# Performance work log

Measured on AMD Instinct MI355X. Metric: run time of the kernel, lower is better.

## Reference

```python
import jax, jax.numpy as jnp
import numpy as np

N_NODES = 50000
N_EDGES = 800000
NODE_IN = 16
EDGE_IN = 3
G_DIM = 8
LATENT = 128
NODE_OUT = 1
EDGE_OUT = 1


def _dense_init(key, fan_in, fan_out):
    # flax default: lecun_normal weights, zero bias
    w = jax.random.normal(key, (fan_in, fan_out), jnp.float32) / jnp.sqrt(float(fan_in))
    b = jnp.zeros((fan_out,), jnp.float32)
    return w, b


def setup_inputs() -> dict:
    key = jax.random.key(0)
    ks = jax.random.split(key, 12)
    nodes = jax.random.normal(ks[0], (N_NODES, NODE_IN), jnp.float32)
    edges = jax.random.normal(ks[1], (N_EDGES, EDGE_IN), jnp.float32)
    globals_ = jax.random.normal(ks[2], (1, G_DIM), jnp.float32)
    senders = jax.random.randint(ks[3], (N_EDGES,), 0, N_NODES, jnp.int32)
    receivers = jax.random.randint(ks[4], (N_EDGES,), 0, N_NODES, jnp.int32)
    W_en, b_en = _dense_init(ks[5], NODE_IN, LATENT)      # encoder node Dense
    W_ee, b_ee = _dense_init(ks[6], EDGE_IN, LATENT)      # encoder edge Dense
    mlp_in = 3 * LATENT + G_DIM                           # concat(nodes, sent, recv, globals)
    W1, b1 = _dense_init(ks[7], mlp_in, LATENT)           # node MLP layer 1 (relu)
    W2, b2 = _dense_init(ks[8], LATENT, LATENT)           # node MLP layer 2
    W_dn, b_dn = _dense_init(ks[9], LATENT, NODE_OUT)     # decoder node Dense
    W_de, b_de = _dense_init(ks[10], LATENT, EDGE_OUT)    # decoder edge Dense
    return dict(nodes=nodes, edges=edges, globals_=globals_, senders=senders,
                receivers=receivers, W_en=W_en, b_en=b_en, W_ee=W_ee, b_ee=b_ee,
                W1=W1, b1=b1, W2=W2, b2=b2, W_dn=W_dn, b_dn=b_dn, W_de=W_de, b_de=b_de)


def reference(nodes, edges, globals_, senders, receivers,
              W_en, b_en, W_ee, b_ee, W1, b1, W2, b2, W_dn, b_dn, W_de, b_de):
    n = nodes.shape[0]
    # Encoder (GraphMapFeatures)
    h_n = nodes @ W_en + b_en                     # [N, L]
    h_e = edges @ W_ee + b_ee                     # [E, L]
    # One jraph.GraphNetwork step, update_edge_fn=None -> edges unchanged.
    # sent/received aggregation = segment_sum of edge features by sender/receiver.
    sent = jax.ops.segment_sum(h_e, senders, num_segments=n)      # [N, L]
    recv = jax.ops.segment_sum(h_e, receivers, num_segments=n)    # [N, L]
    gbc = jnp.broadcast_to(globals_[0], (n, globals_.shape[1]))   # single graph
    x = jnp.concatenate((h_n, sent, recv, gbc), axis=1)           # [N, 3L+G]
    x = jax.nn.relu(x @ W1 + b1)
    h_n = x @ W2 + b2
    # update_global_fn reconstructs concat([time], static) == globals (identity).
    # Decoder
    nodes_out = h_n @ W_dn + b_dn                 # [N, 1]
    edges_out = h_e @ W_de + b_de                 # [E, 1]
    return nodes_out, edges_out
```

## Files before the change

kernel.cpp:

```cpp
#include <hip/hip_runtime.h>

#define N_NODES 50000
#define N_EDGES 800000

#define ESR_OFF    0
#define CONSTS_OFF 400000
#define SCAL_OFF   404096
#define PART_OFF   404608

#define NBINS      25
#define BINSZ      2000
#define MAX_CHUNKS 20

__global__ void precompute_kernel(
    const float* __restrict__ g,
    const float* __restrict__ W_en,
    const float* __restrict__ b_en,
    const float* __restrict__ W_ee,
    const float* __restrict__ b_ee,
    const float* __restrict__ W1,
    const float* __restrict__ b1,
    const float* __restrict__ W2,
    const float* __restrict__ b2,
    const float* __restrict__ W_dn,
    const float* __restrict__ b_dn,
    const float* __restrict__ W_de,
    const float* __restrict__ b_de,
    float* __restrict__ ws)
{
    const int s = blockIdx.x;
    const int k = threadIdx.x;
    float* consts = ws + CONSTS_OFF;
    float* scal   = ws + SCAL_OFF;

    if (s < 16) {
        float acc = 0.f;
        for (int l = 0; l < 128; ++l)
            acc += W_en[s * 128 + l] * W1[l * 128 + k];
        consts[k * 32 + s] = acc;
    } else if (s < 19) {
        const int j = s - 16;
        float acc = 0.f;
        for (int l = 0; l < 128; ++l)
            acc += W_ee[j * 128 + l] * W1[(128 + l) * 128 + k];
        consts[k * 32 + s] = acc;
    } else if (s < 22) {
        const int j = s - 19;
        float acc = 0.f;
        for (int l = 0; l < 128; ++l)
            acc += W_ee[j * 128 + l] * W1[(256 + l) * 128 + k];
        consts[k * 32 + s] = acc;
    } else if (s == 22) {
        float acc = b1[k];
        for (int l = 0; l < 128; ++l)
            acc += b_en[l] * W1[l * 128 + k];
        for (int j = 0; j < 8; ++j)
            acc += g[j] * W1[(384 + j) * 128 + k];
        consts[k * 32 + 22] = acc;
    } else if (s == 23) {
        float acc = 0.f;
        for (int l = 0; l < 128; ++l)
            acc += b_ee[l] * W1[(128 + l) * 128 + k];
        consts[k * 32 + 23] = acc;
    } else if (s == 24) {
        float acc = 0.f;
        for (int l = 0; l < 128; ++l)
            acc += b_ee[l] * W1[(256 + l) * 128 + k];
        consts[k * 32 + 24] = acc;
    } else if (s == 25) {
        float acc = 0.f;
        for (int j = 0; j < 128; ++j)
            acc += W2[k * 128 + j] * W_dn[j];
        consts[k * 32 + 25] = acc;
        consts[k * 32 + 26] = 0.f;
        consts[k * 32 + 27] = 0.f;
    } else {
        if (k == 0) {
            float c = b_dn[0];
            for (int j = 0; j < 128; ++j) c += b2[j] * W_dn[j];
            scal[0] = c;
            float ce = b_de[0];
            for (int l = 0; l < 128; ++l) ce += b_ee[l] * W_de[l];
            scal[1] = ce;
            scal[5] = 0.f; scal[6] = 0.f; scal[7] = 0.f;
        }
        if (k < 3) {
            float acc = 0.f;
            for (int l = 0; l < 128; ++l)
                acc += W_ee[k * 128 + l] * W_de[l];
            scal[2 + k] = acc;
        }
    }
}

__global__ __launch_bounds__(256) void edge_out_kernel(
    const float* __restrict__ edges,
    const float* __restrict__ ws,
    float* __restrict__ out_edges)
{
    const int e4 = (blockIdx.x * 256 + threadIdx.x) * 4;
    if (e4 >= N_EDGES) return;
    const float* scal = ws + SCAL_OFF;
    const float w0 = scal[2], w1 = scal[3], w2 = scal[4], cb = scal[1];
    const float4* ep = (const float4*)(edges + (size_t)e4 * 3);
    const float4 f0 = ep[0], f1 = ep[1], f2 = ep[2];
    float4 o;
    o.x = fmaf(f0.x, w0, fmaf(f0.y, w1, fmaf(f0.z, w2, cb)));
    o.y = fmaf(f0.w, w0, fmaf(f1.x, w1, fmaf(f1.y, w2, cb)));
    o.z = fmaf(f1.z, w0, fmaf(f1.w, w1, fmaf(f2.x, w2, cb)));
    o.w = fmaf(f2.y, w0, fmaf(f2.z, w1, fmaf(f2.w, w2, cb)));
    *(float4*)(out_edges + e4) = o;
}

__global__ __launch_bounds__(512) void agg_kernel(
    const float* __restrict__ edges,
    const int*   __restrict__ senders,
    const int*   __restrict__ receivers,
    float* __restrict__ ws,
    int ce)
{
    __shared__ float4 acc4[BINSZ * 2];
    float* acc = (float*)acc4;
    const int tid = threadIdx.x;
    for (int i = tid; i < BINSZ * 2; i += 512)
        acc4[i] = make_float4(0.f, 0.f, 0.f, 0.f);
    __syncthreads();

    const int chunk = blockIdx.x;
    const int bin   = blockIdx.y;
    const int lo    = bin * BINSZ;

    const int e_beg = chunk * ce;
    const int e_end = min(e_beg + ce, N_EDGES);
    for (int e4 = e_beg + tid * 4; e4 < e_end; e4 += 512 * 4) {
        const int4 s4 = *(const int4*)(senders + e4);
        const int4 r4 = *(const int4*)(receivers + e4);
        const unsigned ds0 = (unsigned)(s4.x - lo), ds1 = (unsigned)(s4.y - lo);
        const unsigned ds2 = (unsigned)(s4.z - lo), ds3 = (unsigned)(s4.w - lo);
        const unsigned dr0 = (unsigned)(r4.x - lo), dr1 = (unsigned)(r4.y - lo);
        const unsigned dr2 = (unsigned)(r4.z - lo), dr3 = (unsigned)(r4.w - lo);
        const bool h = (ds0 < BINSZ) | (ds1 < BINSZ) | (ds2 < BINSZ) | (ds3 < BINSZ) |
                       (dr0 < BINSZ) | (dr1 < BINSZ) | (dr2 < BINSZ) | (dr3 < BINSZ);
        if (!h) continue;
        const float4* ep = (const float4*)(edges + (size_t)e4 * 3);
        const float4 f0 = ep[0], f1 = ep[1], f2 = ep[2];
        if (ds0 < BINSZ) {
            atomicAdd(&acc[ds0 * 8 + 0], f0.x); atomicAdd(&acc[ds0 * 8 + 1], f0.y);
            atomicAdd(&acc[ds0 * 8 + 2], f0.z); atomicAdd(&acc[ds0 * 8 + 3], 1.0f);
        }
        if (dr0 < BINSZ) {
            atomicAdd(&acc[dr0 * 8 + 4], f0.x); atomicAdd(&acc[dr0 * 8 + 5], f0.y);
            atomicAdd(&acc[dr0 * 8 + 6], f0.z); atomicAdd(&acc[dr0 * 8 + 7], 1.0f);
        }
        if (ds1 < BINSZ) {
            atomicAdd(&acc[ds1 * 8 + 0], f0.w); atomicAdd(&acc[ds1 * 8 + 1], f1.x);
            atomicAdd(&acc[ds1 * 8 + 2], f1.y); atomicAdd(&acc[ds1 * 8 + 3], 1.0f);
        }
        if (dr1 < BINSZ) {
            atomicAdd(&acc[dr1 * 8 + 4], f0.w); atomicAdd(&acc[dr1 * 8 + 5], f1.x);
            atomicAdd(&acc[dr1 * 8 + 6], f1.y); atomicAdd(&acc[dr1 * 8 + 7], 1.0f);
        }
        if (ds2 < BINSZ) {
            atomicAdd(&acc[ds2 * 8 + 0], f1.z); atomicAdd(&acc[ds2 * 8 + 1], f1.w);
            atomicAdd(&acc[ds2 * 8 + 2], f2.x); atomicAdd(&acc[ds2 * 8 + 3], 1.0f);
        }
        if (dr2 < BINSZ) {
            atomicAdd(&acc[dr2 * 8 + 4], f1.z); atomicAdd(&acc[dr2 * 8 + 5], f1.w);
            atomicAdd(&acc[dr2 * 8 + 6], f2.x); atomicAdd(&acc[dr2 * 8 + 7], 1.0f);
        }
        if (ds3 < BINSZ) {
            atomicAdd(&acc[ds3 * 8 + 0], f2.y); atomicAdd(&acc[ds3 * 8 + 1], f2.z);
            atomicAdd(&acc[ds3 * 8 + 2], f2.w); atomicAdd(&acc[ds3 * 8 + 3], 1.0f);
        }
        if (dr3 < BINSZ) {
            atomicAdd(&acc[dr3 * 8 + 4], f2.y); atomicAdd(&acc[dr3 * 8 + 5], f2.z);
            atomicAdd(&acc[dr3 * 8 + 6], f2.w); atomicAdd(&acc[dr3 * 8 + 7], 1.0f);
        }
    }
    __syncthreads();

    float4* dst = (float4*)(ws + PART_OFF + (size_t)chunk * (N_NODES * 8) + (size_t)lo * 8);
    for (int i = tid; i < BINSZ * 2; i += 512)
        dst[i] = acc4[i];
}

__global__ __launch_bounds__(256) void edge_kernel_atomic(
    const float* __restrict__ edges,
    const int*   __restrict__ senders,
    const int*   __restrict__ receivers,
    float* __restrict__ ws)
{
    const int e = blockIdx.x * 256 + threadIdx.x;
    if (e >= N_EDGES) return;
    const float e0 = edges[e * 3 + 0];
    const float e1 = edges[e * 3 + 1];
    const float e2 = edges[e * 3 + 2];
    const int s = senders[e];
    const int r = receivers[e];
    float* esr = ws + ESR_OFF;
    atomicAdd(&esr[s * 8 + 0], e0);
    atomicAdd(&esr[s * 8 + 1], e1);
    atomicAdd(&esr[s * 8 + 2], e2);
    atomicAdd(&esr[s * 8 + 3], 1.0f);
    atomicAdd(&esr[r * 8 + 4], e0);
    atomicAdd(&esr[r * 8 + 5], e1);
    atomicAdd(&esr[r * 8 + 6], e2);
    atomicAdd(&esr[r * 8 + 7], 1.0f);
}

__global__ __launch_bounds__(256) void node_kernel(
    const float* __restrict__ nodes,
    const float* __restrict__ ws,
    float* __restrict__ out_nodes,
    int nchunks)
{
    __shared__ float4 lds4[128 * 8];
    const float4* consts4 = (const float4*)(ws + CONSTS_OFF);
    for (int i = threadIdx.x; i < 128 * 8; i += 256)
        lds4[i] = consts4[i];
    __syncthreads();

    const int n = blockIdx.x * 256 + threadIdx.x;
    if (n >= N_NODES) return;

    const float4* np4 = (const float4*)(nodes + (size_t)n * 16);
    const float4 n0 = np4[0], n1 = np4[1], n2 = np4[2], n3 = np4[3];

    float4 es = make_float4(0.f, 0.f, 0.f, 0.f);
    float4 er = make_float4(0.f, 0.f, 0.f, 0.f);
    if (nchunks > 0) {
        for (int c = 0; c < nchunks; ++c) {
            const float4* p = (const float4*)(ws + PART_OFF + (size_t)c * (N_NODES * 8) + (size_t)n * 8);
            const float4 a = p[0], b = p[1];
            es.x += a.x; es.y += a.y; es.z += a.z; es.w += a.w;
            er.x += b.x; er.y += b.y; er.z += b.z; er.w += b.w;
        }
    } else {
        const float4* p = (const float4*)(ws + ESR_OFF + (size_t)n * 8);
        es = p[0];
        er = p[1];
    }

    float acc = 0.f;
#pragma unroll 4
    for (int k = 0; k < 128; ++k) {
        const float4* c4 = &lds4[k * 8];
        const float4 m0 = c4[0], m1 = c4[1], m2 = c4[2], m3 = c4[3];
        const float4 q0 = c4[4];
        const float4 q1 = c4[5];
        const float4 q2 = c4[6];
        float pre = q1.z
            + n0.x * m0.x + n0.y * m0.y + n0.z * m0.z + n0.w * m0.w
            + n1.x * m1.x + n1.y * m1.y + n1.z * m1.z + n1.w * m1.w
            + n2.x * m2.x + n2.y * m2.y + n2.z * m2.z + n2.w * m2.w
            + n3.x * m3.x + n3.y * m3.y + n3.z * m3.z + n3.w * m3.w
            + es.x * q0.x + es.y * q0.y + es.z * q0.z
            + er.x * q0.w + er.y * q1.x + er.z * q1.y
            + es.w * q1.w + er.w * q2.x;
        acc += fmaxf(pre, 0.f) * q2.y;
    }
    const float* scal = ws + SCAL_OFF;
    out_nodes[n] = acc + scal[0];
}

extern "C" void kernel_launch(void* const* d_in, const int* in_sizes, int n_in,
                              void* d_out, int out_size, void* d_ws, size_t ws_size,
                              hipStream_t stream) {
    const float* nodes     = (const float*)d_in[0];
    const float* edges     = (const float*)d_in[1];
    const float* globals_  = (const float*)d_in[2];
    const int*   senders   = (const int*)d_in[3];
    const int*   receivers = (const int*)d_in[4];
    const float* W_en = (const float*)d_in[5];
    const float* b_en = (const float*)d_in[6];
    const float* W_ee = (const float*)d_in[7];
    const float* b_ee = (const float*)d_in[8];
    const float* W1   = (const float*)d_in[9];
    const float* b1   = (const float*)d_in[10];
    const float* W2   = (const float*)d_in[11];
    const float* b2   = (const float*)d_in[12];
    const float* W_dn = (const float*)d_in[13];
    const float* b_dn = (const float*)d_in[14];
    const float* W_de = (const float*)d_in[15];
    const float* b_de = (const float*)d_in[16];

    float* ws = (float*)d_ws;
    float* out = (float*)d_out;

    precompute_kernel<<<27, 128, 0, stream>>>(
        globals_, W_en, b_en, W_ee, b_ee, W1, b1, W2, b2,
        W_dn, b_dn, W_de, b_de, ws);

    edge_out_kernel<<<(N_EDGES / 4 + 255) / 256, 256, 0, stream>>>(
        edges, ws, out + N_NODES);

    long ws_floats = (long)(ws_size / 4);
    long avail = (ws_floats - PART_OFF) / (N_NODES * 8);
    int nchunks = (int)(avail < 0 ? 0 : (avail > MAX_CHUNKS ? MAX_CHUNKS : avail));

    if (nchunks >= 1) {
        int ce = (N_EDGES + nchunks - 1) / nchunks;
        ce = (ce + 3) & ~3;
        dim3 grid(nchunks, NBINS);
        agg_kernel<<<grid, 512, 0, stream>>>(edges, senders, receivers, ws, ce);
    } else {
        hipMemsetAsync(ws + ESR_OFF, 0, (size_t)N_NODES * 8 * sizeof(float), stream);
        edge_kernel_atomic<<<(N_EDGES + 255) / 256, 256, 0, stream>>>(
            edges, senders, receivers, ws);
    }

    node_kernel<<<(N_NODES + 255) / 256, 256, 0, stream>>>(
        nodes, ws, out, nchunks);
}
```

Before: 175.1 us.

## Split aggregation into separate sender and receiver bins with larger LDS bins

The aggregation kernel now gives sender and receiver scatter each their own blocks. Each block reads only one index array and accumulates 4 floats per node instead of 8, which lets a bin cover 4000 nodes in the same LDS footprint. The partial buffers are split into separate sender and receiver arrays, and the per-thread step grows to 8 edges. The point is to cut the number of bins each block must scan and the redundant index reads. In exchange, edge features are now read by both the sender and receiver passes, and the node-range check for the last partial bin has to be handled at write-out.

```diff
diff --git a/kernel.cpp b/kernel.cpp
--- a/kernel.cpp
+++ b/kernel.cpp
@@ -8,8 +8,8 @@
 #define SCAL_OFF   404096
 #define PART_OFF   404608
 
-#define NBINS      25
-#define BINSZ      2000
+#define NBINS      13
+#define BINSZ      4000
 #define MAX_CHUNKS 20
 
 __global__ void precompute_kernel(
@@ -116,71 +116,80 @@
     const float* __restrict__ edges,
     const int*   __restrict__ senders,
     const int*   __restrict__ receivers,
-    float* __restrict__ ws,
+    float* __restrict__ part_s,
+    float* __restrict__ part_r,
     int ce)
 {
-    __shared__ float4 acc4[BINSZ * 2];
+    __shared__ float4 acc4[BINSZ];
     float* acc = (float*)acc4;
     const int tid = threadIdx.x;
-    for (int i = tid; i < BINSZ * 2; i += 512)
+    for (int i = tid; i < BINSZ; i += 512)
         acc4[i] = make_float4(0.f, 0.f, 0.f, 0.f);
     __syncthreads();
 
-    const int chunk = blockIdx.x;
-    const int bin   = blockIdx.y;
-    const int lo    = bin * BINSZ;
+    const int chunk  = blockIdx.x;
+    const int binid  = blockIdx.y;
+    const bool is_s  = binid < NBINS;
+    const int bin    = is_s ? binid : binid - NBINS;
+    const int lo     = bin * BINSZ;
+    const int* __restrict__ idx = is_s ? senders : receivers;
 
     const int e_beg = chunk * ce;
     const int e_end = min(e_beg + ce, N_EDGES);
-    for (int e4 = e_beg + tid * 4; e4 < e_end; e4 += 512 * 4) {
-        const int4 s4 = *(const int4*)(senders + e4);
-        const int4 r4 = *(const int4*)(receivers + e4);
-        const unsigned ds0 = (unsigned)(s4.x - lo), ds1 = (unsigned)(s4.y - lo);
-        const unsigned ds2 = (unsigned)(s4.z - lo), ds3 = (unsigned)(s4.w - lo);
-        const unsigned dr0 = (unsigned)(r4.x - lo), dr1 = (unsigned)(r4.y - lo);
-        const unsigned dr2 = (unsigned)(r4.z - lo), dr3 = (unsigned)(r4.w - lo);
-        const bool h = (ds0 < BINSZ) | (ds1 < BINSZ) | (ds2 < BINSZ) | (ds3 < BINSZ) |
-                       (dr0 < BINSZ) | (dr1 < BINSZ) | (dr2 < BINSZ) | (dr3 < BINSZ);
-        if (!h) continue;
-        const float4* ep = (const float4*)(edges + (size_t)e4 * 3);
-        const float4 f0 = ep[0], f1 = ep[1], f2 = ep[2];
-        if (ds0 < BINSZ) {
-            atomicAdd(&acc[ds0 * 8 + 0], f0.x); atomicAdd(&acc[ds0 * 8 + 1], f0.y);
-            atomicAdd(&acc[ds0 * 8 + 2], f0.z); atomicAdd(&acc[ds0 * 8 + 3], 1.0f);
-        }
-        if (dr0 < BINSZ) {
-            atomicAdd(&acc[dr0 * 8 + 4], f0.x); atomicAdd(&acc[dr0 * 8 + 5], f0.y);
-            atomicAdd(&acc[dr0 * 8 + 6], f0.z); atomicAdd(&acc[dr0 * 8 + 7], 1.0f);
-        }
-        if (ds1 < BINSZ) {
-            atomicAdd(&acc[ds1 * 8 + 0], f0.w); atomicAdd(&acc[ds1 * 8 + 1], f1.x);
-            atomicAdd(&acc[ds1 * 8 + 2], f1.y); atomicAdd(&acc[ds1 * 8 + 3], 1.0f);
-        }
-        if (dr1 < BINSZ) {
-            atomicAdd(&acc[dr1 * 8 + 4], f0.w); atomicAdd(&acc[dr1 * 8 + 5], f1.x);
-            atomicAdd(&acc[dr1 * 8 + 6], f1.y); atomicAdd(&acc[dr1 * 8 + 7], 1.0f);
-        }
-        if (ds2 < BINSZ) {
-            atomicAdd(&acc[ds2 * 8 + 0], f1.z); atomicAdd(&acc[ds2 * 8 + 1], f1.w);
-            atomicAdd(&acc[ds2 * 8 + 2], f2.x); atomicAdd(&acc[ds2 * 8 + 3], 1.0f);
-        }
-        if (dr2 < BINSZ) {
-            atomicAdd(&acc[dr2 * 8 + 4], f1.z); atomicAdd(&acc[dr2 * 8 + 5], f1.w);
-            atomicAdd(&acc[dr2 * 8 + 6], f2.x); atomicAdd(&acc[dr2 * 8 + 7], 1.0f);
-        }
-        if (ds3 < BINSZ) {
-            atomicAdd(&acc[ds3 * 8 + 0], f2.y); atomicAdd(&acc[ds3 * 8 + 1], f2.z);
-            atomicAdd(&acc[ds3 * 8 + 2], f2.w); atomicAdd(&acc[ds3 * 8 + 3], 1.0f);
-        }
-        if (dr3 < BINSZ) {
-            atomicAdd(&acc[dr3 * 8 + 4], f2.y); atomicAdd(&acc[dr3 * 8 + 5], f2.z);
-            atomicAdd(&acc[dr3 * 8 + 6], f2.w); atomicAdd(&acc[dr3 * 8 + 7], 1.0f);
+    for (int e8 = e_beg + tid * 8; e8 < e_end; e8 += 512 * 8) {
+        const int4 ia = *(const int4*)(idx + e8);
+        const int4 ib = *(const int4*)(idx + e8 + 4);
+        const unsigned d0 = (unsigned)(ia.x - lo), d1 = (unsigned)(ia.y - lo);
+        const unsigned d2 = (unsigned)(ia.z - lo), d3 = (unsigned)(ia.w - lo);
+        const unsigned d4 = (unsigned)(ib.x - lo), d5 = (unsigned)(ib.y - lo);
+        const unsigned d6 = (unsigned)(ib.z - lo), d7 = (unsigned)(ib.w - lo);
+        if ((d0 < BINSZ) | (d1 < BINSZ) | (d2 < BINSZ) | (d3 < BINSZ)) {
+            const float4* ep = (const float4*)(edges + (size_t)e8 * 3);
+            const float4 f0 = ep[0], f1 = ep[1], f2 = ep[2];
+            if (d0 < BINSZ) {
+                atomicAdd(&acc[d0 * 4 + 0], f0.x); atomicAdd(&acc[d0 * 4 + 1], f0.y);
+                atomicAdd(&acc[d0 * 4 + 2], f0.z); atomicAdd(&acc[d0 * 4 + 3], 1.0f);
+            }
+            if (d1 < BINSZ) {
+                atomicAdd(&acc[d1 * 4 + 0], f0.w); atomicAdd(&acc[d1 * 4 + 1], f1.x);
+                atomicAdd(&acc[d1 * 4 + 2], f1.y); atomicAdd(&acc[d1 * 4 + 3], 1.0f);
+            }
+            if (d2 < BINSZ) {
+                atomicAdd(&acc[d2 * 4 + 0], f1.z); atomicAdd(&acc[d2 * 4 + 1], f1.w);
+                atomicAdd(&acc[d2 * 4 + 2], f2.x); atomicAdd(&acc[d2 * 4 + 3], 1.0f);
+            }
+            if (d3 < BINSZ) {
+                atomicAdd(&acc[d3 * 4 + 0], f2.y); atomicAdd(&acc[d3 * 4 + 1], f2.z);
+                atomicAdd(&acc[d3 * 4 + 2], f2.w); atomicAdd(&acc[d3 * 4 + 3], 1.0f);
+            }
+        }
+        if ((d4 < BINSZ) | (d5 < BINSZ) | (d6 < BINSZ) | (d7 < BINSZ)) {
+            const float4* ep = (const float4*)(edges + (size_t)e8 * 3 + 12);
+            const float4 f0 = ep[0], f1 = ep[1], f2 = ep[2];
+            if (d4 < BINSZ) {
+                atomicAdd(&acc[d4 * 4 + 0], f0.x); atomicAdd(&acc[d4 * 4 + 1], f0.y);
+                atomicAdd(&acc[d4 * 4 + 2], f0.z); atomicAdd(&acc[d4 * 4 + 3], 1.0f);
+            }
+            if (d5 < BINSZ) {
+                atomicAdd(&acc[d5 * 4 + 0], f0.w); atomicAdd(&acc[d5 * 4 + 1], f1.x);
+                atomicAdd(&acc[d5 * 4 + 2], f1.y); atomicAdd(&acc[d5 * 4 + 3], 1.0f);
+            }
+            if (d6 < BINSZ) {
+                atomicAdd(&acc[d6 * 4 + 0], f1.z); atomicAdd(&acc[d6 * 4 + 1], f1.w);
+                atomicAdd(&acc[d6 * 4 + 2], f2.x); atomicAdd(&acc[d6 * 4 + 3], 1.0f);
+            }
+            if (d7 < BINSZ) {
+                atomicAdd(&acc[d7 * 4 + 0], f2.y); atomicAdd(&acc[d7 * 4 + 1], f2.z);
+                atomicAdd(&acc[d7 * 4 + 2], f2.w); atomicAdd(&acc[d7 * 4 + 3], 1.0f);
+            }
         }
     }
     __syncthreads();
 
-    float4* dst = (float4*)(ws + PART_OFF + (size_t)chunk * (N_NODES * 8) + (size_t)lo * 8);
-    for (int i = tid; i < BINSZ * 2; i += 512)
+    float* base = (is_s ? part_s : part_r) + (size_t)chunk * (N_NODES * 4) + (size_t)lo * 4;
+    const int lim = min(BINSZ, N_NODES - lo);
+    float4* dst = (float4*)base;
+    for (int i = tid; i < lim; i += 512)
         dst[i] = acc4[i];
 }
 
@@ -211,6 +220,8 @@
 __global__ __launch_bounds__(256) void node_kernel(
     const float* __restrict__ nodes,
     const float* __restrict__ ws,
+    const float* __restrict__ part_s,
+    const float* __restrict__ part_r,
     float* __restrict__ out_nodes,
     int nchunks)
 {
@@ -230,8 +241,8 @@
     float4 er = make_float4(0.f, 0.f, 0.f, 0.f);
     if (nchunks > 0) {
         for (int c = 0; c < nchunks; ++c) {
-            const float4* p = (const float4*)(ws + PART_OFF + (size_t)c * (N_NODES * 8) + (size_t)n * 8);
-            const float4 a = p[0], b = p[1];
+            const float4 a = *(const float4*)(part_s + (size_t)c * (N_NODES * 4) + (size_t)n * 4);
+            const float4 b = *(const float4*)(part_r + (size_t)c * (N_NODES * 4) + (size_t)n * 4);
             es.x += a.x; es.y += a.y; es.z += a.z; es.w += a.w;
             er.x += b.x; er.y += b.y; er.z += b.z; er.w += b.w;
         }
@@ -295,14 +306,19 @@
         edges, ws, out + N_NODES);
 
     long ws_floats = (long)(ws_size / 4);
-    long avail = (ws_floats - PART_OFF) / (N_NODES * 8);
+    long per_chunk = 2L * N_NODES * 4;
+    long avail = (ws_floats - PART_OFF) / per_chunk;
     int nchunks = (int)(avail < 0 ? 0 : (avail > MAX_CHUNKS ? MAX_CHUNKS : avail));
+
+    float* part_s = ws + PART_OFF;
+    float* part_r = part_s + (size_t)nchunks * (N_NODES * 4);
 
     if (nchunks >= 1) {
         int ce = (N_EDGES + nchunks - 1) / nchunks;
-        ce = (ce + 3) & ~3;
-        dim3 grid(nchunks, NBINS);
-        agg_kernel<<<grid, 512, 0, stream>>>(edges, senders, receivers, ws, ce);
+        ce = (ce + 7) & ~7;
+        dim3 grid(nchunks, 2 * NBINS);
+        agg_kernel<<<grid, 512, 0, stream>>>(
+            edges, senders, receivers, part_s, part_r, ce);
     } else {
         hipMemsetAsync(ws + ESR_OFF, 0, (size_t)N_NODES * 8 * sizeof(float), stream);
         edge_kernel_atomic<<<(N_EDGES + 255) / 256, 256, 0, stream>>>(
@@ -310,5 +326,5 @@
     }
 
     node_kernel<<<(N_NODES + 255) / 256, 256, 0, stream>>>(
-        nodes, ws, out, nchunks);
-}
+        nodes, ws, part_s, part_r, out, nchunks);
+}
```

Measured after the change: 177.6 us. Within noise of the previous version (+1.4%).
